# Optimization experiments

Measured on AMD Instinct MI355X. Metric: run time of the kernel, lower is better.

Reference implementation:

```python
import jax, jax.numpy as jnp
import numpy as np

L, B, T = 2, 32, 64
H, E, V = 1024, 512, 32000


def setup_inputs() -> dict:
    key = jax.random.key(0)
    ks = jax.random.split(key, 10)
    s = 0.02  # small init scale so sigmoid/tanh stay in a sane range
    return {
        "X": jax.random.randint(ks[0], (B, T), 0, V, dtype=jnp.int64),
        "h0": jax.random.normal(ks[1], (L, B, H), jnp.float32) * 0.1,
        "emb": jax.random.normal(ks[2], (V, E), jnp.float32) * s,
        "W0": jax.random.normal(ks[3], (E + H, 3 * H), jnp.float32) * s,
        "U0": jax.random.normal(ks[4], (H, 3 * H), jnp.float32) * s,
        "b0": jnp.zeros((2, 3 * H), jnp.float32),
        "W1": jax.random.normal(ks[5], (H, 3 * H), jnp.float32) * s,
        "U1": jax.random.normal(ks[6], (H, 3 * H), jnp.float32) * s,
        "b1": jnp.zeros((2, 3 * H), jnp.float32),
        "Wd": jax.random.normal(ks[7], (H, V), jnp.float32) * s,
        "bd": jnp.zeros((V,), jnp.float32),
    }


def gru_cell(x, h, W, U, b):
    # Keras GRUCell, reset_after=True; gate order: z (update), r (reset), h (new)
    gx = x @ W + b[0]          # [B, 3H]
    gh = h @ U + b[1]          # [B, 3H]
    xz, xr, xh = jnp.split(gx, 3, axis=-1)
    hz, hr, hh = jnp.split(gh, 3, axis=-1)
    z = jax.nn.sigmoid(xz + hz)
    r = jax.nn.sigmoid(xr + hr)
    hcand = jnp.tanh(xh + r * hh)
    return z * h + (1.0 - z) * hcand


def reference(X, h0, emb, W0, U0, b0, W1, U1, b1, Wd, bd):
    Xe = emb[X]                                  # [B, T, E]
    context = h0[-1]                             # [B, H], last-layer initial state
    dec_in = jnp.concatenate(
        [Xe, jnp.broadcast_to(context[:, None, :], (B, T, H))], axis=-1
    )                                            # [B, T, E+H]

    def step(carry, x_t):
        h1, h2 = carry
        h1 = gru_cell(x_t, h1, W0, U0, b0)
        h2 = gru_cell(h1, h2, W1, U1, b1)
        return (h1, h2), h2

    (h1T, h2T), seq = jax.lax.scan(step, (h0[0], h0[1]), jnp.swapaxes(dec_in, 0, 1))
    seq = jnp.swapaxes(seq, 0, 1)                # [B, T, H]
    logits = seq @ Wd + bd                       # [B, T, V]
    return logits, jnp.stack([h1T, h2T], axis=0)
```

## Files before the change

kernel.cpp:

```cpp
#include <hip/hip_runtime.h>
#include <hip/hip_bf16.h>

typedef __bf16 bf16_t;
typedef __bf16 bf16x8 __attribute__((ext_vector_type(8)));
typedef float f32x4 __attribute__((ext_vector_type(4)));
typedef unsigned u32x4 __attribute__((ext_vector_type(4)));

#define MFMA16x16x32(a, b, c) __builtin_amdgcn_mfma_f32_16x16x32_bf16((a), (b), (c), 0, 0, 0)

#define B_ 32
#define T_ 64
#define H_ 1024
#define E_ 512
#define V_ 32000
#define H3 3072
#define MROWS 2048
#define LOGITS_SZ ((size_t)MROWS * V_)

__device__ __forceinline__ u32x4 ld16_sc1(const void* p) {
  u32x4 v;
  asm volatile("global_load_dwordx4 %0, %1, off sc1" : "=v"(v) : "v"(p));
  return v;
}
__device__ __forceinline__ float ldf_sc1(const float* p) {
  float v;
  asm volatile("global_load_dword %0, %1, off sc1" : "=v"(v) : "v"(p));
  return v;
}
__device__ __forceinline__ void st_bf16_agent(bf16_t* p, float x) {
  bf16_t h = (bf16_t)x;
  unsigned short u = __builtin_bit_cast(unsigned short, h);
  __hip_atomic_store((unsigned short*)p, u, __ATOMIC_RELAXED, __HIP_MEMORY_SCOPE_AGENT);
}
__device__ __forceinline__ void stf_agent(float* p, float x) {
  __hip_atomic_store(p, x, __ATOMIC_RELAXED, __HIP_MEMORY_SCOPE_AGENT);
}

__global__ __launch_bounds__(256) void k_transpose_bf16(
    const float* __restrict__ in, bf16_t* __restrict__ out, int R, int C) {
  __shared__ float tile[32][33];
  int c0 = blockIdx.x * 32, r0 = blockIdx.y * 32;
  int tx = threadIdx.x & 31, ty = threadIdx.x >> 5;
#pragma unroll
  for (int i = 0; i < 4; ++i) {
    int r = ty + i * 8;
    tile[r][tx] = in[(size_t)(r0 + r) * C + (c0 + tx)];
  }
  __syncthreads();
#pragma unroll
  for (int i = 0; i < 4; ++i) {
    int r = ty + i * 8;
    out[(size_t)(c0 + r) * R + (r0 + tx)] = (bf16_t)tile[tx][r];
  }
}

__global__ __launch_bounds__(256) void k_build_A0(
    const int* __restrict__ X, const float* __restrict__ emb,
    const float* __restrict__ h0, bf16_t* __restrict__ A0) {
  int idx = blockIdx.x * 256 + threadIdx.x;
  int row = idx / (E_ + H_);
  int c = idx - row * (E_ + H_);
  float v;
  if (c < E_) {
    int tok = X[row];
    v = emb[(size_t)tok * E_ + c];
  } else {
    int b = row >> 6;
    v = h0[(size_t)B_ * H_ + (size_t)b * H_ + (c - E_)];
  }
  A0[idx] = (bf16_t)v;
}

__global__ __launch_bounds__(256) void k_init_h(
    const float* __restrict__ h0, float* __restrict__ h1f, bf16_t* __restrict__ h1b,
    float* __restrict__ h2f, bf16_t* __restrict__ h2b, unsigned* __restrict__ bar) {
  int i = blockIdx.x * 256 + threadIdx.x;
  if (i == 0) bar[0] = 0u;
  float a = h0[i], b = h0[B_ * H_ + i];
  h1f[i] = a; h1b[i] = (bf16_t)a;
  h2f[i] = b; h2b[i] = (bf16_t)b;
}

__global__ __launch_bounds__(256) void k_gemm(
    const bf16_t* __restrict__ A, const bf16_t* __restrict__ BT,
    const float* __restrict__ bias, float* __restrict__ out,
    int M, int N, int K) {
  __shared__ bf16_t Asm[64][40];
  __shared__ bf16_t Bsm[64][40];
  int tid = threadIdx.x;
  int m0 = blockIdx.x * 64, n0 = blockIdx.y * 64;
  int lane = tid & 63, w = tid >> 6;
  int lr = lane & 15, q = lane >> 4;
  int wm = w & 1, wn = w >> 1;
  int srow = tid >> 2, sseg = (tid & 3) * 8;
  f32x4 acc[2][2] = {};
  const bf16_t* Ap = A + (size_t)(m0 + srow) * K + sseg;
  const bf16_t* Bp = BT + (size_t)(n0 + srow) * K + sseg;
  for (int kc = 0; kc < K; kc += 32) {
    *(bf16x8*)&Asm[srow][sseg] = *(const bf16x8*)(Ap + kc);
    *(bf16x8*)&Bsm[srow][sseg] = *(const bf16x8*)(Bp + kc);
    __syncthreads();
#pragma unroll
    for (int sm = 0; sm < 2; ++sm) {
      bf16x8 af = *(const bf16x8*)&Asm[wm * 32 + sm * 16 + lr][q * 8];
#pragma unroll
      for (int sn = 0; sn < 2; ++sn) {
        bf16x8 bfr = *(const bf16x8*)&Bsm[wn * 32 + sn * 16 + lr][q * 8];
        acc[sm][sn] = MFMA16x16x32(af, bfr, acc[sm][sn]);
      }
    }
    __syncthreads();
  }
#pragma unroll
  for (int sm = 0; sm < 2; ++sm)
#pragma unroll
    for (int sn = 0; sn < 2; ++sn) {
      int gr = m0 + wm * 32 + sm * 16 + q * 4;
      int gc = n0 + wn * 32 + sn * 16 + lr;
      float bb = bias[gc];
#pragma unroll
      for (int r = 0; r < 4; ++r)
        out[(size_t)(gr + r) * N + gc] = acc[sm][sn][r] + bb;
    }
}

struct RecurArgs {
  const bf16_t *U0T, *W1T, *U1T;
  const float *gx0, *b0h, *b1x, *b1h;
  float *h1f, *h2f, *gx1;
  bf16_t *h1b0, *h1b1, *h2b0, *h2b1, *seqb;
  unsigned* bar;
};

__global__ __launch_bounds__(384) void k_recur(RecurArgs a) {
  extern __shared__ char smem[];
  char* sm_w = smem;
  char* sm_s = smem + 98304;
  const int tid = threadIdx.x;
  const int lane = tid & 63;
  const int u = tid >> 6;
  const int wm = u & 1, g = u >> 1;
  const int lr = lane & 15, q = lane >> 4;
  const int blk = blockIdx.x;
  const int grp = blk >> 6;
  const int ig = blk & 63;
  const int i = ig * 16 + lr;

  {
    const bf16_t* wsrc = (grp == 0) ? a.U0T : (grp == 1) ? a.W1T : a.U1T;
    int rr = tid >> 3, c0 = tid & 7;
    int wg = rr >> 4, wl = rr & 15;
    const char* srow = (const char*)(wsrc + ((size_t)wg * 1024 + (size_t)ig * 16 + wl) * 1024);
    char* drow = sm_w + (size_t)rr * 2048;
    int sw = rr & 7;
#pragma unroll
    for (int j = 0; j < 16; ++j) {
      int gk = c0 + 8 * j;
      *(u32x4*)(drow + (size_t)((gk ^ sw) * 16)) = *(const u32x4*)(srow + (size_t)gk * 16);
    }
  }
  __syncthreads();

  float bz = 0.f, br = 0.f, bh3 = 0.f, bxz = 0.f, bxr = 0.f, bxh = 0.f;
  if (grp == 0) { bz = a.b0h[i]; br = a.b0h[H_ + i]; bh3 = a.b0h[2 * H_ + i]; }
  if (grp == 2) {
    bz = a.b1h[i]; br = a.b1h[H_ + i]; bh3 = a.b1h[2 * H_ + i];
    bxz = a.b1x[i]; bxr = a.b1x[H_ + i]; bxh = a.b1x[2 * H_ + i];
  }

  const int swl = lr & 7;
  const char* arow = sm_s + (size_t)(wm * 16 + lr) * 2048;
  const char* wrow = sm_w + (size_t)(g * 16 + lr) * 2048;

  for (int ph = 0; ph < 66; ++ph) {
    int t = (grp == 0) ? ph : (grp == 1) ? (ph - 1) : (ph - 2);
    bool act = (t >= 0) && (t < 64);
    if (act) {
      int par = ph & 1;
      const bf16_t* hsrc = (grp == 2) ? (par ? a.h2b1 : a.h2b0)
                                      : (par ? a.h1b1 : a.h1b0);
      u32x4 tmp[16];
      float xv0[4], xv1[4], xv2[4];
      if (tid < 256) {
        int sb = tid >> 3, c0 = tid & 7;
        const char* src = (const char*)hsrc + (size_t)sb * 2048 + (size_t)c0 * 16;
#pragma unroll
        for (int j = 0; j < 16; ++j) tmp[j] = ld16_sc1(src + (size_t)j * 128);
      }
      if (grp == 2 && u < 2) {
        const float* gxb = a.gx1 + (size_t)(t & 1) * 32 * H3;
#pragma unroll
        for (int r = 0; r < 4; ++r) {
          int b = wm * 16 + q * 4 + r;
          const float* pb = gxb + (size_t)b * H3 + i;
          xv0[r] = ldf_sc1(pb);
          xv1[r] = ldf_sc1(pb + 1024);
          xv2[r] = ldf_sc1(pb + 2048);
        }
      } else if (grp == 0 && u < 2) {
#pragma unroll
        for (int r = 0; r < 4; ++r) {
          int b = wm * 16 + q * 4 + r;
          const float* gx = a.gx0 + (size_t)(b * T_ + t) * H3;
          xv0[r] = gx[i]; xv1[r] = gx[H_ + i]; xv2[r] = gx[2 * H_ + i];
        }
      }
      asm volatile("s_waitcnt vmcnt(0)" ::: "memory");
      __builtin_amdgcn_sched_barrier(0);
      if (tid < 256) {
        int sb = tid >> 3, c0 = tid & 7;
        char* dst = sm_s + (size_t)sb * 2048;
        int sw = sb & 7;
#pragma unroll
        for (int j = 0; j < 16; ++j) {
          int gk = c0 + 8 * j;
          *(u32x4*)(dst + (size_t)((gk ^ sw) * 16)) = tmp[j];
        }
      }
      __syncthreads();

      f32x4 acc = {0.f, 0.f, 0.f, 0.f};
#pragma unroll 4
      for (int kc = 0; kc < 32; ++kc) {
        int gi = kc * 4 + q;
        bf16x8 af = *(const bf16x8*)(arow + (size_t)((gi ^ swl) * 16));
        bf16x8 wf = *(const bf16x8*)(wrow + (size_t)((gi ^ swl) * 16));
        acc = MFMA16x16x32(af, wf, acc);
      }

      if (grp == 1) {
        float* go = a.gx1 + (size_t)(t & 1) * 32 * H3;
#pragma unroll
        for (int r = 0; r < 4; ++r) {
          int b = wm * 16 + q * 4 + r;
          stf_agent(go + (size_t)b * H3 + (size_t)g * 1024 + i, acc[r]);
        }
      } else {
        __syncthreads();
        char* scr = sm_s;
        if (g >= 1)
          *(f32x4*)(scr + (size_t)((((g - 1) * 2 + wm) * 64 + lane) * 16)) = acc;
        __syncthreads();
        if (g == 0) {
          f32x4 rgv = *(const f32x4*)(scr + (size_t)(((0 * 2 + wm) * 64 + lane) * 16));
          f32x4 hgv = *(const f32x4*)(scr + (size_t)(((1 * 2 + wm) * 64 + lane) * 16));
          if (grp == 0) {
            bf16_t* h1bn = par ? a.h1b0 : a.h1b1;
#pragma unroll
            for (int r = 0; r < 4; ++r) {
              int b = wm * 16 + q * 4 + r;
              float z  = 1.f / (1.f + __expf(-(xv0[r] + acc[r] + bz)));
              float rg = 1.f / (1.f + __expf(-(xv1[r] + rgv[r] + br)));
              float hc = tanhf(xv2[r] + rg * (hgv[r] + bh3));
              float hold = a.h1f[b * H_ + i];
              float hn = z * hold + (1.f - z) * hc;
              a.h1f[b * H_ + i] = hn;
              st_bf16_agent(&h1bn[b * H_ + i], hn);
            }
          } else {
            bf16_t* h2bn = par ? a.h2b0 : a.h2b1;
#pragma unroll
            for (int r = 0; r < 4; ++r) {
              int b = wm * 16 + q * 4 + r;
              float z  = 1.f / (1.f + __expf(-(xv0[r] + bxz + acc[r] + bz)));
              float rg = 1.f / (1.f + __expf(-(xv1[r] + bxr + rgv[r] + br)));
              float hc = tanhf(xv2[r] + bxh + rg * (hgv[r] + bh3));
              float hold = a.h2f[b * H_ + i];
              float hn = z * hold + (1.f - z) * hc;
              a.h2f[b * H_ + i] = hn;
              st_bf16_agent(&h2bn[b * H_ + i], hn);
              a.seqb[(size_t)(b * T_ + t) * H_ + i] = (bf16_t)hn;
            }
          }
        }
      }
    }
    if (ph < 65) {
      __syncthreads();
      if (tid == 0) {
        __hip_atomic_fetch_add(a.bar, 1u, __ATOMIC_RELAXED, __HIP_MEMORY_SCOPE_AGENT);
        unsigned tgt = 192u * (unsigned)(ph + 1);
        while (__hip_atomic_load(a.bar, __ATOMIC_RELAXED, __HIP_MEMORY_SCOPE_AGENT) < tgt)
          __builtin_amdgcn_s_sleep(1);
      }
      __syncthreads();
    }
  }
}

__global__ __launch_bounds__(256) void k_final(
    const float* __restrict__ h1f, const float* __restrict__ h2f,
    float* __restrict__ out) {
  int i = blockIdx.x * 256 + threadIdx.x;
  out[LOGITS_SZ + i] = h1f[i];
  out[LOGITS_SZ + B_ * H_ + i] = h2f[i];
}

extern "C" void kernel_launch(void* const* d_in, const int* in_sizes, int n_in,
                              void* d_out, int out_size, void* d_ws, size_t ws_size,
                              hipStream_t stream) {
  const int*   X   = (const int*)d_in[0];
  const float* h0  = (const float*)d_in[1];
  const float* emb = (const float*)d_in[2];
  const float* W0  = (const float*)d_in[3];
  const float* U0  = (const float*)d_in[4];
  const float* b0  = (const float*)d_in[5];
  const float* W1  = (const float*)d_in[6];
  const float* U1  = (const float*)d_in[7];
  const float* b1  = (const float*)d_in[8];
  const float* Wd  = (const float*)d_in[9];
  const float* bd  = (const float*)d_in[10];
  float* out = (float*)d_out;

  char* p = (char*)d_ws;
  bf16_t* W0T = (bf16_t*)p; p += (size_t)H3 * (E_ + H_) * 2;
  bf16_t* U0T = (bf16_t*)p; p += (size_t)H3 * H_ * 2;
  bf16_t* W1T = (bf16_t*)p; p += (size_t)H3 * H_ * 2;
  bf16_t* U1T = (bf16_t*)p; p += (size_t)H3 * H_ * 2;
  bf16_t* WdT = (bf16_t*)p; p += (size_t)V_ * H_ * 2;
  bf16_t* A0  = (bf16_t*)p; p += (size_t)MROWS * (E_ + H_) * 2;
  bf16_t* seqb = (bf16_t*)p; p += (size_t)MROWS * H_ * 2;
  float* gx0 = (float*)p; p += (size_t)MROWS * H3 * 4;
  float* h1f = (float*)p; p += B_ * H_ * 4;
  float* h1f_unused = (float*)p; p += B_ * H_ * 4;
  float* h2f = (float*)p; p += B_ * H_ * 4;
  float* h2f_unused = (float*)p; p += B_ * H_ * 4;
  bf16_t* h1b0 = (bf16_t*)p; p += B_ * H_ * 2;
  bf16_t* h1b1 = (bf16_t*)p; p += B_ * H_ * 2;
  bf16_t* h2b0 = (bf16_t*)p; p += B_ * H_ * 2;
  bf16_t* h2b1 = (bf16_t*)p; p += B_ * H_ * 2;
  unsigned* bar = (unsigned*)p; p += 128;
  (void)h1f_unused; (void)h2f_unused;
  float* gx1 = (float*)A0;

  k_transpose_bf16<<<dim3(H3 / 32, (E_ + H_) / 32), 256, 0, stream>>>(W0, W0T, E_ + H_, H3);
  k_transpose_bf16<<<dim3(H3 / 32, H_ / 32), 256, 0, stream>>>(U0, U0T, H_, H3);
  k_transpose_bf16<<<dim3(H3 / 32, H_ / 32), 256, 0, stream>>>(W1, W1T, H_, H3);
  k_transpose_bf16<<<dim3(H3 / 32, H_ / 32), 256, 0, stream>>>(U1, U1T, H_, H3);
  k_transpose_bf16<<<dim3(V_ / 32, H_ / 32), 256, 0, stream>>>(Wd, WdT, H_, V_);

  k_build_A0<<<(MROWS * (E_ + H_)) / 256, 256, 0, stream>>>(X, emb, h0, A0);
  k_init_h<<<(B_ * H_) / 256, 256, 0, stream>>>(h0, h1f, h1b0, h2f, h2b0, bar);

  k_gemm<<<dim3(MROWS / 64, H3 / 64), 256, 0, stream>>>(A0, W0T, b0, gx0, MROWS, H3, E_ + H_);

  RecurArgs ra;
  ra.U0T = U0T; ra.W1T = W1T; ra.U1T = U1T;
  ra.gx0 = gx0; ra.b0h = b0 + H3; ra.b1x = b1; ra.b1h = b1 + H3;
  ra.h1f = h1f; ra.h2f = h2f; ra.gx1 = gx1;
  ra.h1b0 = h1b0; ra.h1b1 = h1b1; ra.h2b0 = h2b0; ra.h2b1 = h2b1;
  ra.seqb = seqb; ra.bar = bar;
  static int lds_opted = 0;
  if (!lds_opted) {
    hipFuncSetAttribute((const void*)k_recur,
                        hipFuncAttributeMaxDynamicSharedMemorySize, 163840);
    lds_opted = 1;
  }
  void* kargs[] = {&ra};
  hipLaunchCooperativeKernel((const void*)k_recur, dim3(192), dim3(384), kargs,
                             163840, stream);

  k_gemm<<<dim3(MROWS / 64, V_ / 64), 256, 0, stream>>>(seqb, WdT, bd, out, MROWS, V_, H_);

  k_final<<<(B_ * H_) / 256, 256, 0, stream>>>(h1f, h2f, out);
}
```

Baseline: 1.448 ms.

## Retile GEMMs to 128x128 with direct-to-LDS loads, flag barrier, transposed gx1

The GEMM kernel now computes 128x128 tiles with a 4x4 grid of MFMA accumulators per wave. It loads operands straight into LDS with global_load_lds, which raises operand reuse and removes register staging. In the recurrence, the layer-1 input gates are stored batch-contiguous so each lane reads and writes them with one 16-byte access instead of several scalar ones. The single atomic-counter grid barrier is replaced by per-block padded flags that waiting threads poll in parallel. The trade-offs are higher register pressure and an unpadded LDS layout that may cause bank conflicts in the GEMM, plus more polling traffic at the barrier.

```diff
diff --git a/kernel.cpp b/kernel.cpp
--- a/kernel.cpp
+++ b/kernel.cpp
@@ -16,24 +16,38 @@
 #define H3 3072
 #define MROWS 2048
 #define LOGITS_SZ ((size_t)MROWS * V_)
+#define NBLK 192
+#define FLAG_STRIDE 16
 
 __device__ __forceinline__ u32x4 ld16_sc1(const void* p) {
   u32x4 v;
   asm volatile("global_load_dwordx4 %0, %1, off sc1" : "=v"(v) : "v"(p));
   return v;
 }
-__device__ __forceinline__ float ldf_sc1(const float* p) {
-  float v;
-  asm volatile("global_load_dword %0, %1, off sc1" : "=v"(v) : "v"(p));
-  return v;
+__device__ __forceinline__ f32x4 ld16f_sc1(const void* p) {
+  u32x4 v;
+  asm volatile("global_load_dwordx4 %0, %1, off sc1" : "=v"(v) : "v"(p));
+  return __builtin_bit_cast(f32x4, v);
+}
+__device__ __forceinline__ void st16_sc1(void* p, f32x4 v) {
+  asm volatile("global_store_dwordx4 %0, %1, off sc1" :: "v"(p), "v"(v) : "memory");
 }
 __device__ __forceinline__ void st_bf16_agent(bf16_t* p, float x) {
   bf16_t h = (bf16_t)x;
   unsigned short u = __builtin_bit_cast(unsigned short, h);
   __hip_atomic_store((unsigned short*)p, u, __ATOMIC_RELAXED, __HIP_MEMORY_SCOPE_AGENT);
 }
-__device__ __forceinline__ void stf_agent(float* p, float x) {
-  __hip_atomic_store(p, x, __ATOMIC_RELAXED, __HIP_MEMORY_SCOPE_AGENT);
+__device__ __forceinline__ void st_u32_agent(unsigned* p, unsigned v) {
+  __hip_atomic_store(p, v, __ATOMIC_RELAXED, __HIP_MEMORY_SCOPE_AGENT);
+}
+__device__ __forceinline__ unsigned ld_u32_agent(const unsigned* p) {
+  return __hip_atomic_load(p, __ATOMIC_RELAXED, __HIP_MEMORY_SCOPE_AGENT);
+}
+
+__device__ __forceinline__ void gld_lds16(const bf16_t* g, bf16_t* l) {
+  __builtin_amdgcn_global_load_lds(
+      (const __attribute__((address_space(1))) unsigned*)g,
+      (__attribute__((address_space(3))) unsigned*)l, 16, 0, 0);
 }
 
 __global__ __launch_bounds__(256) void k_transpose_bf16(
@@ -73,9 +87,9 @@
 
 __global__ __launch_bounds__(256) void k_init_h(
     const float* __restrict__ h0, float* __restrict__ h1f, bf16_t* __restrict__ h1b,
-    float* __restrict__ h2f, bf16_t* __restrict__ h2b, unsigned* __restrict__ bar) {
+    float* __restrict__ h2f, bf16_t* __restrict__ h2b, unsigned* __restrict__ flags) {
   int i = blockIdx.x * 256 + threadIdx.x;
-  if (i == 0) bar[0] = 0u;
+  if (i < NBLK * FLAG_STRIDE) flags[i] = 0u;
   float a = h0[i], b = h0[B_ * H_ + i];
   h1f[i] = a; h1b[i] = (bf16_t)a;
   h2f[i] = b; h2b[i] = (bf16_t)b;
@@ -85,38 +99,46 @@
     const bf16_t* __restrict__ A, const bf16_t* __restrict__ BT,
     const float* __restrict__ bias, float* __restrict__ out,
     int M, int N, int K) {
-  __shared__ bf16_t Asm[64][40];
-  __shared__ bf16_t Bsm[64][40];
+  __shared__ bf16_t Asm[128 * 32];
+  __shared__ bf16_t Bsm[128 * 32];
   int tid = threadIdx.x;
-  int m0 = blockIdx.x * 64, n0 = blockIdx.y * 64;
+  int m0 = blockIdx.x * 128, n0 = blockIdx.y * 128;
   int lane = tid & 63, w = tid >> 6;
   int lr = lane & 15, q = lane >> 4;
-  int wm = w & 1, wn = w >> 1;
-  int srow = tid >> 2, sseg = (tid & 3) * 8;
-  f32x4 acc[2][2] = {};
-  const bf16_t* Ap = A + (size_t)(m0 + srow) * K + sseg;
-  const bf16_t* Bp = BT + (size_t)(n0 + srow) * K + sseg;
+  int wr = w >> 1, wc = w & 1;
+  int srow = lane >> 2, scol = (lane & 3) * 8;
+  const bf16_t* Ag = A + (size_t)(m0 + w * 32 + srow) * K + scol;
+  const bf16_t* Bg = BT + (size_t)(n0 + w * 32 + srow) * K + scol;
+  bf16_t* Ald = Asm + (size_t)(w * 32) * 32;
+  bf16_t* Bld = Bsm + (size_t)(w * 32) * 32;
+  f32x4 acc[4][4] = {};
   for (int kc = 0; kc < K; kc += 32) {
-    *(bf16x8*)&Asm[srow][sseg] = *(const bf16x8*)(Ap + kc);
-    *(bf16x8*)&Bsm[srow][sseg] = *(const bf16x8*)(Bp + kc);
+    gld_lds16(Ag + kc, Ald);
+    gld_lds16(Ag + (size_t)16 * K + kc, Ald + 16 * 32);
+    gld_lds16(Bg + kc, Bld);
+    gld_lds16(Bg + (size_t)16 * K + kc, Bld + 16 * 32);
+    asm volatile("s_waitcnt vmcnt(0)" ::: "memory");
     __syncthreads();
-#pragma unroll
-    for (int sm = 0; sm < 2; ++sm) {
-      bf16x8 af = *(const bf16x8*)&Asm[wm * 32 + sm * 16 + lr][q * 8];
-#pragma unroll
-      for (int sn = 0; sn < 2; ++sn) {
-        bf16x8 bfr = *(const bf16x8*)&Bsm[wn * 32 + sn * 16 + lr][q * 8];
-        acc[sm][sn] = MFMA16x16x32(af, bfr, acc[sm][sn]);
-      }
-    }
+    bf16x8 af[4], bfr[4];
+#pragma unroll
+    for (int sm = 0; sm < 4; ++sm)
+      af[sm] = *(const bf16x8*)&Asm[(size_t)(wr * 64 + sm * 16 + lr) * 32 + q * 8];
+#pragma unroll
+    for (int sn = 0; sn < 4; ++sn)
+      bfr[sn] = *(const bf16x8*)&Bsm[(size_t)(wc * 64 + sn * 16 + lr) * 32 + q * 8];
+#pragma unroll
+    for (int sm = 0; sm < 4; ++sm)
+#pragma unroll
+      for (int sn = 0; sn < 4; ++sn)
+        acc[sm][sn] = MFMA16x16x32(af[sm], bfr[sn], acc[sm][sn]);
     __syncthreads();
   }
 #pragma unroll
-  for (int sm = 0; sm < 2; ++sm)
-#pragma unroll
-    for (int sn = 0; sn < 2; ++sn) {
-      int gr = m0 + wm * 32 + sm * 16 + q * 4;
-      int gc = n0 + wn * 32 + sn * 16 + lr;
+  for (int sm = 0; sm < 4; ++sm)
+#pragma unroll
+    for (int sn = 0; sn < 4; ++sn) {
+      int gr = m0 + wr * 64 + sm * 16 + q * 4;
+      int gc = n0 + wc * 64 + sn * 16 + lr;
       float bb = bias[gc];
 #pragma unroll
       for (int r = 0; r < 4; ++r)
@@ -127,9 +149,9 @@
 struct RecurArgs {
   const bf16_t *U0T, *W1T, *U1T;
   const float *gx0, *b0h, *b1x, *b1h;
-  float *h1f, *h2f, *gx1;
+  float *h1f, *h2f, *gx1t;
   bf16_t *h1b0, *h1b1, *h2b0, *h2b1, *seqb;
-  unsigned* bar;
+  unsigned* flags;
 };
 
 __global__ __launch_bounds__(384) void k_recur(RecurArgs a) {
@@ -180,7 +202,7 @@
       const bf16_t* hsrc = (grp == 2) ? (par ? a.h2b1 : a.h2b0)
                                       : (par ? a.h1b1 : a.h1b0);
       u32x4 tmp[16];
-      float xv0[4], xv1[4], xv2[4];
+      f32x4 xv0, xv1, xv2;
       if (tid < 256) {
         int sb = tid >> 3, c0 = tid & 7;
         const char* src = (const char*)hsrc + (size_t)sb * 2048 + (size_t)c0 * 16;
@@ -188,15 +210,11 @@
         for (int j = 0; j < 16; ++j) tmp[j] = ld16_sc1(src + (size_t)j * 128);
       }
       if (grp == 2 && u < 2) {
-        const float* gxb = a.gx1 + (size_t)(t & 1) * 32 * H3;
-#pragma unroll
-        for (int r = 0; r < 4; ++r) {
-          int b = wm * 16 + q * 4 + r;
-          const float* pb = gxb + (size_t)b * H3 + i;
-          xv0[r] = ldf_sc1(pb);
-          xv1[r] = ldf_sc1(pb + 1024);
-          xv2[r] = ldf_sc1(pb + 2048);
-        }
+        const float* gxb = a.gx1t + (size_t)(t & 1) * H3 * 32;
+        int boff = wm * 16 + q * 4;
+        xv0 = ld16f_sc1(gxb + (size_t)i * 32 + boff);
+        xv1 = ld16f_sc1(gxb + (size_t)(1024 + i) * 32 + boff);
+        xv2 = ld16f_sc1(gxb + (size_t)(2048 + i) * 32 + boff);
       } else if (grp == 0 && u < 2) {
 #pragma unroll
         for (int r = 0; r < 4; ++r) {
@@ -229,12 +247,8 @@
       }
 
       if (grp == 1) {
-        float* go = a.gx1 + (size_t)(t & 1) * 32 * H3;
-#pragma unroll
-        for (int r = 0; r < 4; ++r) {
-          int b = wm * 16 + q * 4 + r;
-          stf_agent(go + (size_t)b * H3 + (size_t)g * 1024 + i, acc[r]);
-        }
+        float* go = a.gx1t + (size_t)(t & 1) * H3 * 32;
+        st16_sc1(go + (size_t)(g * 1024 + i) * 32 + wm * 16 + q * 4, acc);
       } else {
         __syncthreads();
         char* scr = sm_s;
@@ -276,12 +290,13 @@
       }
     }
     if (ph < 65) {
+      asm volatile("s_waitcnt vmcnt(0)" ::: "memory");
       __syncthreads();
-      if (tid == 0) {
-        __hip_atomic_fetch_add(a.bar, 1u, __ATOMIC_RELAXED, __HIP_MEMORY_SCOPE_AGENT);
-        unsigned tgt = 192u * (unsigned)(ph + 1);
-        while (__hip_atomic_load(a.bar, __ATOMIC_RELAXED, __HIP_MEMORY_SCOPE_AGENT) < tgt)
-          __builtin_amdgcn_s_sleep(1);
+      if (tid == 0) st_u32_agent(&a.flags[blk * FLAG_STRIDE], (unsigned)(ph + 1));
+      if (tid < NBLK) {
+        unsigned tgt = (unsigned)(ph + 1);
+        while (ld_u32_agent(&a.flags[tid * FLAG_STRIDE]) < tgt)
+          __builtin_amdgcn_s_sleep(2);
       }
       __syncthreads();
     }
@@ -322,16 +337,15 @@
   bf16_t* seqb = (bf16_t*)p; p += (size_t)MROWS * H_ * 2;
   float* gx0 = (float*)p; p += (size_t)MROWS * H3 * 4;
   float* h1f = (float*)p; p += B_ * H_ * 4;
-  float* h1f_unused = (float*)p; p += B_ * H_ * 4;
+  unsigned* flags = (unsigned*)p; p += B_ * H_ * 4;
   float* h2f = (float*)p; p += B_ * H_ * 4;
   float* h2f_unused = (float*)p; p += B_ * H_ * 4;
   bf16_t* h1b0 = (bf16_t*)p; p += B_ * H_ * 2;
   bf16_t* h1b1 = (bf16_t*)p; p += B_ * H_ * 2;
   bf16_t* h2b0 = (bf16_t*)p; p += B_ * H_ * 2;
   bf16_t* h2b1 = (bf16_t*)p; p += B_ * H_ * 2;
-  unsigned* bar = (unsigned*)p; p += 128;
-  (void)h1f_unused; (void)h2f_unused;
-  float* gx1 = (float*)A0;
+  (void)h2f_unused;
+  float* gx1t = (float*)A0;
 
   k_transpose_bf16<<<dim3(H3 / 32, (E_ + H_) / 32), 256, 0, stream>>>(W0, W0T, E_ + H_, H3);
   k_transpose_bf16<<<dim3(H3 / 32, H_ / 32), 256, 0, stream>>>(U0, U0T, H_, H3);
@@ -340,16 +354,16 @@
   k_transpose_bf16<<<dim3(V_ / 32, H_ / 32), 256, 0, stream>>>(Wd, WdT, H_, V_);
 
   k_build_A0<<<(MROWS * (E_ + H_)) / 256, 256, 0, stream>>>(X, emb, h0, A0);
-  k_init_h<<<(B_ * H_) / 256, 256, 0, stream>>>(h0, h1f, h1b0, h2f, h2b0, bar);
-
-  k_gemm<<<dim3(MROWS / 64, H3 / 64), 256, 0, stream>>>(A0, W0T, b0, gx0, MROWS, H3, E_ + H_);
+  k_init_h<<<(B_ * H_) / 256, 256, 0, stream>>>(h0, h1f, h1b0, h2f, h2b0, flags);
+
+  k_gemm<<<dim3(MROWS / 128, H3 / 128), 256, 0, stream>>>(A0, W0T, b0, gx0, MROWS, H3, E_ + H_);
 
   RecurArgs ra;
   ra.U0T = U0T; ra.W1T = W1T; ra.U1T = U1T;
   ra.gx0 = gx0; ra.b0h = b0 + H3; ra.b1x = b1; ra.b1h = b1 + H3;
-  ra.h1f = h1f; ra.h2f = h2f; ra.gx1 = gx1;
+  ra.h1f = h1f; ra.h2f = h2f; ra.gx1t = gx1t;
   ra.h1b0 = h1b0; ra.h1b1 = h1b1; ra.h2b0 = h2b0; ra.h2b1 = h2b1;
-  ra.seqb = seqb; ra.bar = bar;
+  ra.seqb = seqb; ra.flags = flags;
   static int lds_opted = 0;
   if (!lds_opted) {
     hipFuncSetAttribute((const void*)k_recur,
@@ -357,10 +371,10 @@
     lds_opted = 1;
   }
   void* kargs[] = {&ra};
-  hipLaunchCooperativeKernel((const void*)k_recur, dim3(192), dim3(384), kargs,
+  hipLaunchCooperativeKernel((const void*)k_recur, dim3(NBLK), dim3(384), kargs,
                              163840, stream);
 
-  k_gemm<<<dim3(MROWS / 64, V_ / 64), 256, 0, stream>>>(seqb, WdT, bd, out, MROWS, V_, H_);
+  k_gemm<<<dim3(MROWS / 128, V_ / 128), 256, 0, stream>>>(seqb, WdT, bd, out, MROWS, V_, H_);
 
   k_final<<<(B_ * H_) / 256, 256, 0, stream>>>(h1f, h2f, out);
 }
```

Result: faster. 1.164 ms (-19.6%).
